# Kernel tuning notes

Hardware: AMD Instinct MI355X
Metric: run time of the kernel (lower is better)

Reference implementation:

```python
import jax, jax.numpy as jnp
import numpy as np

B, T = 256, 512
N_POS, N_ACT, H = 128, 64, 512
I = N_POS + N_ACT  # 192


def setup_inputs() -> dict:
    key = jax.random.key(0)
    ks = jax.random.split(key, 10)
    return {
        "observation": jax.random.normal(ks[0], (B, T, N_POS), jnp.float32),
        "action": jax.random.normal(ks[1], (B, T, N_ACT), jnp.float32),
        "h0": jax.random.normal(ks[2], (B, H), jnp.float32),
        "c0": jax.random.normal(ks[3], (B, H), jnp.float32),
        "W_ih": jax.random.normal(ks[4], (4 * H, I), jnp.float32) * 0.05,
        "W_hh": jax.random.normal(ks[5], (4 * H, H), jnp.float32) * 0.05,
        "b_ih": jax.random.normal(ks[6], (4 * H,), jnp.float32) * 0.05,
        "b_hh": jax.random.normal(ks[7], (4 * H,), jnp.float32) * 0.05,
        "W_out": jax.random.normal(ks[8], (1, H), jnp.float32) * 0.05,
        "b_out": jax.random.normal(ks[9], (1,), jnp.float32) * 0.05,
    }


def reference(observation, action, h0, c0, W_ih, W_hh, b_ih, b_hh, W_out, b_out):
    # x_t = cat([obs, act], -1): [B, T, I]
    x = jnp.concatenate([observation, action], axis=-1)
    # Precompute input-to-gate projection for all timesteps: [T, B, 4H]
    xg = jnp.swapaxes(jnp.einsum("bti,gi->btg", x, W_ih) + b_ih + b_hh, 0, 1)

    def step(carry, xg_t):
        h, c = carry
        gates = xg_t + h @ W_hh.T  # [B, 4H]
        i, f, g, o = jnp.split(gates, 4, axis=-1)  # PyTorch LSTMCell gate order
        i = jax.nn.sigmoid(i)
        f = jax.nn.sigmoid(f)
        g = jnp.tanh(g)
        o = jax.nn.sigmoid(o)
        c_new = f * c + i * g
        h_new = o * jnp.tanh(c_new)
        return (h_new, c_new), h_new

    (_, _), hs = jax.lax.scan(step, (h0, c0), xg)  # hs: [T, B, H]
    out = jnp.einsum("tbh,oh->tbo", hs, W_out) + b_out  # [T, B, 1]
    return jnp.swapaxes(out, 0, 1)  # [B, T, 1]
```

## Files before the change

### kernel.cpp

```cpp
#include <hip/hip_runtime.h>
#include <hip/hip_bf16.h>
#include <stdint.h>

#define BDIM 512

constexpr int Bb   = 256;
constexpr int Tt   = 512;
constexpr int Hh   = 512;
constexpr int NPOS = 128, NACT = 64, INPD = 192;
constexpr int NGRP = 8;
constexpr int BBr  = 32;
constexpr int NBLK = 32;
constexpr int HHd  = 16;
constexpr int KITH = Hh / 32;
constexpr int KITX = INPD / 32;
constexpr int HPAD = Hh + 8;
constexpr int XPAD = INPD + 8;
constexpr int GPAD = 68;

typedef __attribute__((ext_vector_type(8))) short short8;
typedef __attribute__((ext_vector_type(4))) float f32x4;
typedef __attribute__((ext_vector_type(4))) unsigned int u32x4;

__device__ __forceinline__ float bf2f(unsigned short u) {
  union { unsigned int i; float f; } v; v.i = ((unsigned int)u) << 16; return v.f;
}
__device__ __forceinline__ unsigned short f2bf(float f) {
  __hip_bfloat16 h = __float2bfloat16(f);
  return *reinterpret_cast<unsigned short*>(&h);
}
__device__ __forceinline__ float sigm(float x) { return 1.0f / (1.0f + __expf(-x)); }
__device__ __forceinline__ float tanh_fast(float x) {
  return 1.0f - 2.0f / (1.0f + __expf(2.0f * x));
}

__device__ __forceinline__ void store_wt16(void* p, u32x4 v) {
  asm volatile("global_store_dwordx4 %0, %1, off sc0 sc1" :: "v"(p), "v"(v) : "memory");
}
__device__ __forceinline__ u32x4 load_wt16(const void* p) {
  u32x4 r;
  asm volatile("global_load_dwordx4 %0, %1, off sc0 sc1" : "=v"(r) : "v"(p) : "memory");
  return r;
}
__device__ __forceinline__ void store_wt2(void* p, unsigned short v) {
  unsigned int w = v;
  asm volatile("global_store_short %0, %1, off sc0 sc1" :: "v"(p), "v"(w) : "memory");
}
__device__ __forceinline__ void store_wt4(void* p, unsigned int v) {
  asm volatile("global_store_dword %0, %1, off sc0 sc1" :: "v"(p), "v"(v) : "memory");
}
__device__ __forceinline__ unsigned int load_wt4(const void* p) {
  unsigned int r;
  asm volatile("global_load_dword %0, %1, off sc0 sc1" : "=v"(r) : "v"(p) : "memory");
  return r;
}
__device__ __forceinline__ void waitvm0() {
  asm volatile("s_waitcnt vmcnt(0)" ::: "memory");
}

__global__ void __launch_bounds__(BDIM, 2)
lstm_kernel(const float* __restrict__ obs, const float* __restrict__ actn,
            const float* __restrict__ h0, const float* __restrict__ c0,
            const float* __restrict__ W_ih, const float* __restrict__ W_hh,
            const float* __restrict__ b_ih, const float* __restrict__ b_hh,
            const float* __restrict__ W_out, const float* __restrict__ b_out,
            float* __restrict__ out, unsigned short* __restrict__ hbuf,
            unsigned int* __restrict__ flags)
{
  __shared__ __align__(16) unsigned short h_s[BBr * HPAD];
  __shared__ __align__(16) unsigned short x_s[BBr * XPAD];
  __shared__ float gates_s[BBr * GPAD];
  __shared__ float c_s[BBr * HHd];
  __shared__ float wout_s[Hh];
  __shared__ float bias_s[64];

  const int tid  = threadIdx.x;
  const int g    = blockIdx.x & 7;
  const int jb   = blockIdx.x >> 3;
  const int wv   = tid >> 6, lane = tid & 63;
  const int wm   = wv >> 2;
  const int wn   = wv & 3;
  const int cl   = lane & 15, qd = lane >> 4;

  unsigned short* hb0 = hbuf;
  unsigned short* hb1 = hbuf + (size_t)Bb * Hh;
  const size_t slotbase = (size_t)(g * NBLK + jb) * (BBr * HHd);
  const size_t grpbase  = (size_t)g * NBLK * (BBr * HHd);
  unsigned int* myflag = flags + (size_t)(g * NBLK + jb) * 32;
  const unsigned int* pollflag = flags + (size_t)(g * NBLK + (lane & 31)) * 32;

  short8 wfrag[KITH + KITX];
  {
    const int R = wn * Hh + jb * HHd + cl;
    const float* whh = W_hh + (size_t)R * Hh;
    const float* wih = W_ih + (size_t)R * INPD;
    #pragma unroll
    for (int kk = 0; kk < KITH + KITX; ++kk) {
      const int k0 = kk * 32 + qd * 8;
      short8 s;
      #pragma unroll
      for (int e = 0; e < 8; ++e) {
        const int k = k0 + e;
        const float f = (k < Hh) ? whh[k] : wih[k - Hh];
        s[e] = (short)f2bf(f);
      }
      wfrag[kk] = s;
    }
  }

  if (tid < 64) {
    const int R = (tid >> 4) * Hh + jb * HHd + (tid & 15);
    bias_s[tid] = b_ih[R] + b_hh[R];
  }
  for (int i = tid; i < Hh; i += BDIM) wout_s[i] = W_out[i];
  {
    const int m = tid >> 4, r = tid & 15;
    const size_t gi = (size_t)(g * BBr + m) * Hh + jb * HHd + r;
    c_s[tid] = c0[gi];
    store_wt2(hb0 + slotbase + tid, f2bf(h0[gi]));
  }
  const float bout = b_out[0];

  auto stage_x = [&](int t) {
    #pragma unroll
    for (int it = 0; it < 2; ++it) {
      const int i = tid + BDIM * it;
      const int m = i >> 5, c4 = i & 31;
      const float4 v = *(const float4*)(obs + ((size_t)(g * BBr + m) * Tt + t) * NPOS + c4 * 4);
      uint2 p;
      p.x = (unsigned)f2bf(v.x) | ((unsigned)f2bf(v.y) << 16);
      p.y = (unsigned)f2bf(v.z) | ((unsigned)f2bf(v.w) << 16);
      *(uint2*)(&x_s[m * XPAD + c4 * 4]) = p;
    }
    {
      const int m = tid >> 4, c4 = tid & 15;
      const float4 v = *(const float4*)(actn + ((size_t)(g * BBr + m) * Tt + t) * NACT + c4 * 4);
      uint2 p;
      p.x = (unsigned)f2bf(v.x) | ((unsigned)f2bf(v.y) << 16);
      p.y = (unsigned)f2bf(v.z) | ((unsigned)f2bf(v.w) << 16);
      *(uint2*)(&x_s[m * XPAD + NPOS + c4 * 4]) = p;
    }
  };
  auto xacc_compute = [&]() -> f32x4 {
    f32x4 a;
    { const float bv = bias_s[wn * 16 + cl]; a = (f32x4){bv, bv, bv, bv}; }
    const unsigned short* xrow = &x_s[(wm * 16 + cl) * XPAD + qd * 8];
    #pragma unroll
    for (int j = 0; j < KITX; ++j)
      a = __builtin_amdgcn_mfma_f32_16x16x32_bf16(*(const short8*)(xrow + j * 32),
                                                  wfrag[KITH + j], a, 0, 0, 0);
    return a;
  };
  auto poll = [&](unsigned int tgt) {
    if (tid < 64) {
      int spins = 0;
      for (;;) {
        const unsigned int v = load_wt4(pollflag);
        waitvm0();
        if (__all((int)(v >= tgt))) break;
        if (++spins > 3000000) break;
      }
    }
    __syncthreads();
  };

  waitvm0();
  __syncthreads();
  if (tid == 0) store_wt4(myflag, 1u);
  stage_x(0);
  __syncthreads();
  f32x4 xacc = xacc_compute();
  poll(1u);

  for (int t = 0; t < Tt; ++t) {
    const unsigned short* hsrc = (t & 1) ? hb1 : hb0;
    unsigned short* hdst       = (t & 1) ? hb0 : hb1;

    u32x4 hv[4];
    #pragma unroll
    for (int it = 0; it < 4; ++it) {
      const int i = tid + BDIM * it;
      hv[it] = load_wt16(hsrc + grpbase + (size_t)i * 8);
    }
    waitvm0();
    #pragma unroll
    for (int it = 0; it < 4; ++it) {
      const int i = tid + BDIM * it;
      *(u32x4*)(&h_s[((i >> 1) & 31) * HPAD + (i >> 6) * 16 + (i & 1) * 8]) = hv[it];
    }
    __syncthreads();

    f32x4 acc = xacc;
    const unsigned short* arow = &h_s[(wm * 16 + cl) * HPAD + qd * 8];
    #pragma unroll
    for (int kk = 0; kk < KITH; ++kk)
      acc = __builtin_amdgcn_mfma_f32_16x16x32_bf16(*(const short8*)(arow + kk * 32),
                                                    wfrag[kk], acc, 0, 0, 0);
    #pragma unroll
    for (int rg = 0; rg < 4; ++rg)
      gates_s[(wm * 16 + qd * 4 + rg) * GPAD + wn * 16 + cl] = acc[rg];
    __syncthreads();

    {
      const int m = tid >> 4, r = tid & 15;
      const float gi = gates_s[m * GPAD + r];
      const float gf = gates_s[m * GPAD + 16 + r];
      const float gg = gates_s[m * GPAD + 32 + r];
      const float go = gates_s[m * GPAD + 48 + r];
      const float cp = c_s[tid];
      const float iv = sigm(gi), fv = sigm(gf);
      const float gv = tanh_fast(gg), ov = sigm(go);
      const float cn = fv * cp + iv * gv;
      const float hn = ov * tanh_fast(cn);
      c_s[tid] = cn;
      store_wt2(hdst + slotbase + tid, f2bf(hn));
    }
    waitvm0();
    __syncthreads();
    if (tid == 0) store_wt4(myflag, (unsigned int)(t + 2));

    if (jb == 0 && t > 0 && tid < 256) {
      const int m = tid >> 3, l8 = tid & 7;
      const unsigned short* hr = &h_s[m * HPAD + l8 * 64];
      const float* wr = &wout_s[l8 * 64];
      float sum = 0.f;
      #pragma unroll 8
      for (int e = 0; e < 64; ++e) sum += bf2f(hr[e]) * wr[e];
      sum += __shfl_down(sum, 4, 64);
      sum += __shfl_down(sum, 2, 64);
      sum += __shfl_down(sum, 1, 64);
      if (l8 == 0) out[(size_t)(g * BBr + m) * Tt + (t - 1)] = sum + bout;
    }
    if (t + 1 < Tt) {
      stage_x(t + 1);
      __syncthreads();
      xacc = xacc_compute();
    } else {
      __syncthreads();
    }

    poll((unsigned int)(t + 2));
  }

  if (jb == 0 && tid < 256) {
    const int m = tid >> 3, l8 = tid & 7;
    u32x4 hvv[8];
    #pragma unroll
    for (int it = 0; it < 8; ++it) {
      const size_t a = grpbase + (size_t)((l8 * 4 + (it >> 1)) * BBr + m) * HHd + (it & 1) * 8;
      hvv[it] = load_wt16(hb0 + a);
    }
    waitvm0();
    float sum = 0.f;
    #pragma unroll
    for (int it = 0; it < 8; ++it) {
      const int d0 = l8 * 64 + (it >> 1) * 16 + (it & 1) * 8;
      #pragma unroll
      for (int j = 0; j < 4; ++j) {
        const unsigned u = hvv[it][j];
        sum += bf2f((unsigned short)(u & 0xffffu)) * wout_s[d0 + j * 2];
        sum += bf2f((unsigned short)(u >> 16))     * wout_s[d0 + j * 2 + 1];
      }
    }
    sum += __shfl_down(sum, 4, 64);
    sum += __shfl_down(sum, 2, 64);
    sum += __shfl_down(sum, 1, 64);
    if (l8 == 0) out[(size_t)(g * BBr + m) * Tt + (Tt - 1)] = sum + bout;
  }
}

extern "C" void kernel_launch(void* const* d_in, const int* in_sizes, int n_in,
                              void* d_out, int out_size, void* d_ws, size_t ws_size,
                              hipStream_t stream) {
  const float* obs   = (const float*)d_in[0];
  const float* actn  = (const float*)d_in[1];
  const float* h0    = (const float*)d_in[2];
  const float* c0    = (const float*)d_in[3];
  const float* W_ih  = (const float*)d_in[4];
  const float* W_hh  = (const float*)d_in[5];
  const float* b_ih  = (const float*)d_in[6];
  const float* b_hh  = (const float*)d_in[7];
  const float* W_out = (const float*)d_in[8];
  const float* b_out = (const float*)d_in[9];
  float* out = (float*)d_out;

  unsigned short* hbuf = (unsigned short*)d_ws;
  const size_t hbytes = (size_t)2 * Bb * Hh * sizeof(unsigned short);
  unsigned int* flags = (unsigned int*)((char*)d_ws + hbytes);

  hipMemsetAsync(flags, 0, 256 * 32 * sizeof(unsigned int), stream);

  hipFuncSetAttribute((const void*)lstm_kernel,
                      hipFuncAttributeMaxDynamicSharedMemorySize, 28672);
  hipLaunchKernelGGL(lstm_kernel, dim3(256), dim3(BDIM), 28672, stream,
                     obs, actn, h0, c0, W_ih, W_hh, b_ih, b_hh, W_out, b_out,
                     out, hbuf, flags);
}
```

Measured before the change: 1.944 ms.

## Regroup LSTM blocks per XCD and exchange hidden state through L2

Each block reads its XCC id and takes a rank from an atomic counter, so every batch group of 16 rows is spread over the 16 blocks on the same XCD. That allows hidden-state exchange and flag polling to use L2-coherent (sc0) accesses in place of device-scope ones. A token handshake at startup checks that the group really shares an L2 and falls back to device-scope accesses if not. Blocks now cover 16 batch rows by 32 hidden units, load x straight from global memory into MFMA fragments, and pack h stores into dwords. The cost is extra startup synchronisation and a reliance on how blocks are placed across XCDs.

New measurement: 2.587 ms. 33.1% more time.

```diff
diff --git a/kernel.cpp b/kernel.cpp
--- a/kernel.cpp
+++ b/kernel.cpp
@@ -8,15 +8,14 @@
 constexpr int Tt   = 512;
 constexpr int Hh   = 512;
 constexpr int NPOS = 128, NACT = 64, INPD = 192;
-constexpr int NGRP = 8;
-constexpr int BBr  = 32;
-constexpr int NBLK = 32;
-constexpr int HHd  = 16;
+constexpr int GBLK = 16;
+constexpr int RR   = 16;
+constexpr int HHd  = 32;
 constexpr int KITH = Hh / 32;
 constexpr int KITX = INPD / 32;
+constexpr int KIT  = KITH + KITX;
 constexpr int HPAD = Hh + 8;
-constexpr int XPAD = INPD + 8;
-constexpr int GPAD = 68;
+constexpr int GPAD = 132;
 
 typedef __attribute__((ext_vector_type(8))) short short8;
 typedef __attribute__((ext_vector_type(4))) float f32x4;
@@ -34,25 +33,35 @@
   return 1.0f - 2.0f / (1.0f + __expf(2.0f * x));
 }
 
-__device__ __forceinline__ void store_wt16(void* p, u32x4 v) {
-  asm volatile("global_store_dwordx4 %0, %1, off sc0 sc1" :: "v"(p), "v"(v) : "memory");
-}
-__device__ __forceinline__ u32x4 load_wt16(const void* p) {
+__device__ __forceinline__ u32x4 load_l2_16(const void* p) {
+  u32x4 r;
+  asm volatile("global_load_dwordx4 %0, %1, off sc0" : "=v"(r) : "v"(p) : "memory");
+  return r;
+}
+__device__ __forceinline__ unsigned int load_l2_4(const void* p) {
+  unsigned int r;
+  asm volatile("global_load_dword %0, %1, off sc0" : "=v"(r) : "v"(p) : "memory");
+  return r;
+}
+__device__ __forceinline__ void store_l2_4(void* p, unsigned int v) {
+  asm volatile("global_store_dword %0, %1, off sc0" :: "v"(p), "v"(v) : "memory");
+}
+__device__ __forceinline__ u32x4 load_dev16(const void* p) {
   u32x4 r;
   asm volatile("global_load_dwordx4 %0, %1, off sc0 sc1" : "=v"(r) : "v"(p) : "memory");
   return r;
 }
-__device__ __forceinline__ void store_wt2(void* p, unsigned short v) {
-  unsigned int w = v;
-  asm volatile("global_store_short %0, %1, off sc0 sc1" :: "v"(p), "v"(w) : "memory");
-}
-__device__ __forceinline__ void store_wt4(void* p, unsigned int v) {
-  asm volatile("global_store_dword %0, %1, off sc0 sc1" :: "v"(p), "v"(v) : "memory");
-}
-__device__ __forceinline__ unsigned int load_wt4(const void* p) {
+__device__ __forceinline__ unsigned int load_dev4(const void* p) {
   unsigned int r;
   asm volatile("global_load_dword %0, %1, off sc0 sc1" : "=v"(r) : "v"(p) : "memory");
   return r;
+}
+__device__ __forceinline__ void store_dev4(void* p, unsigned int v) {
+  asm volatile("global_store_dword %0, %1, off sc0 sc1" :: "v"(p), "v"(v) : "memory");
+}
+__device__ __forceinline__ void store_dev2(void* p, unsigned short v) {
+  unsigned int w = v;
+  asm volatile("global_store_short %0, %1, off sc0 sc1" :: "v"(p), "v"(w) : "memory");
 }
 __device__ __forceinline__ void waitvm0() {
   asm volatile("s_waitcnt vmcnt(0)" ::: "memory");
@@ -65,37 +74,112 @@
             const float* __restrict__ b_ih, const float* __restrict__ b_hh,
             const float* __restrict__ W_out, const float* __restrict__ b_out,
             float* __restrict__ out, unsigned short* __restrict__ hbuf,
-            unsigned int* __restrict__ flags)
+            unsigned int* __restrict__ flags, unsigned int* __restrict__ rankcnt,
+            unsigned int* __restrict__ grpbad, unsigned int* __restrict__ tok)
 {
-  __shared__ __align__(16) unsigned short h_s[BBr * HPAD];
-  __shared__ __align__(16) unsigned short x_s[BBr * XPAD];
-  __shared__ float gates_s[BBr * GPAD];
-  __shared__ float c_s[BBr * HHd];
+  __shared__ __align__(16) unsigned short h_s[RR * HPAD];
+  __shared__ float gates_s[RR * GPAD];
+  __shared__ float c_s[RR * HHd];
   __shared__ float wout_s[Hh];
-  __shared__ float bias_s[64];
+  __shared__ float bias_s[4 * HHd];
+  __shared__ int rank_sh;
+  __shared__ int okA_sh, okB_sh, dev_sh;
 
   const int tid  = threadIdx.x;
-  const int g    = blockIdx.x & 7;
-  const int jb   = blockIdx.x >> 3;
   const int wv   = tid >> 6, lane = tid & 63;
-  const int wm   = wv >> 2;
-  const int wn   = wv & 3;
   const int cl   = lane & 15, qd = lane >> 4;
+
+  unsigned int xcc;
+  asm volatile("s_getreg_b32 %0, hwreg(HW_REG_XCC_ID)" : "=s"(xcc));
+  xcc &= 7u;
+  if (tid == 0)
+    rank_sh = (int)__hip_atomic_fetch_add(rankcnt + (size_t)xcc * 32, 1u,
+                                          __ATOMIC_RELAXED, __HIP_MEMORY_SCOPE_AGENT);
+  __syncthreads();
+  const int rank = rank_sh;
+  const int g    = ((int)xcc * 2 + (rank >> 4)) & 15;
+  const int jb   = rank & 15;
 
   unsigned short* hb0 = hbuf;
   unsigned short* hb1 = hbuf + (size_t)Bb * Hh;
-  const size_t slotbase = (size_t)(g * NBLK + jb) * (BBr * HHd);
-  const size_t grpbase  = (size_t)g * NBLK * (BBr * HHd);
-  unsigned int* myflag = flags + (size_t)(g * NBLK + jb) * 32;
-  const unsigned int* pollflag = flags + (size_t)(g * NBLK + (lane & 31)) * 32;
-
-  short8 wfrag[KITH + KITX];
+  const size_t slotbase = (size_t)(g * GBLK + jb) * (RR * HHd);
+  const size_t grpbase  = (size_t)g * GBLK * (RR * HHd);
+  unsigned int* myflag = flags + (size_t)(g * GBLK + jb) * 32;
+  const unsigned int* pollflag = flags + (size_t)(g * GBLK + (lane & 15)) * 32;
+  unsigned int* mytok = tok + (size_t)(g * GBLK + jb) * 32;
+  const unsigned int TOKA = 0xA5000000u | (unsigned)(g << 8) | (unsigned)jb;
+  const unsigned int TOKB = 0x5A000000u | (unsigned)(g << 8) | (unsigned)jb;
+
+  auto pollv = [&](unsigned int tgt, bool dv, int valve) {
+    if (tid < 64) {
+      int spins = 0;
+      for (;;) {
+        const unsigned int v = dv ? load_dev4(pollflag) : load_l2_4(pollflag);
+        waitvm0();
+        if (__all((int)(v >= tgt))) break;
+        if (++spins > valve) break;
+      }
+    }
+    __syncthreads();
+  };
+  auto verify_read = [&](unsigned int expbase) -> void {
+    if (tid < 64) {
+      int good = 1;
+      if (lane < 16) {
+        const unsigned int v = load_l2_4(tok + (size_t)(g * GBLK + lane) * 32);
+        waitvm0();
+        good = (v == (expbase | (unsigned)(g << 8) | (unsigned)lane)) ? 1 : 0;
+      }
+      const int allg = __all(good);
+      if (lane == 0) { if (expbase == 0xA5000000u) okA_sh = allg; else okB_sh = allg; }
+    }
+  };
+
+  if (tid == 0) store_l2_4(mytok, TOKA);
   {
-    const int R = wn * Hh + jb * HHd + cl;
+    const int m = tid >> 5, r = tid & 31;
+    const size_t gi = (size_t)(g * RR + m) * Hh + jb * HHd + r;
+    c_s[tid] = c0[gi];
+    store_dev2(hb0 + slotbase + tid, f2bf(h0[gi]));
+  }
+  waitvm0();
+  __syncthreads();
+  if (tid == 0) store_dev4(myflag, 1u);
+  pollv(1u, true, 2000000);
+  verify_read(0xA5000000u);
+  __syncthreads();
+  if (tid == 0) store_dev4(myflag, 2u);
+  pollv(2u, true, 2000000);
+  if (tid == 0) {
+    store_l2_4(mytok, TOKB);
+    waitvm0();
+    store_dev4(myflag, 3u);
+  }
+  pollv(3u, true, 2000000);
+  verify_read(0x5A000000u);
+  __syncthreads();
+  if (tid == 0) {
+    if (!(okA_sh && okB_sh)) atomicOr(grpbad + (size_t)g * 32, 1u);
+    waitvm0();
+    store_dev4(myflag, 4u);
+  }
+  pollv(4u, true, 2000000);
+  if (tid == 0) {
+    const unsigned int gb = load_dev4(grpbad + (size_t)g * 32);
+    waitvm0();
+    dev_sh = (gb != 0);
+  }
+  __syncthreads();
+  const bool dev = (dev_sh != 0);
+
+  short8 wfrag[KIT];
+  {
+    const int L = wv * 16 + cl, q = L >> 5, r = L & 31;
+    const int R = q * Hh + jb * HHd + r;
     const float* whh = W_hh + (size_t)R * Hh;
     const float* wih = W_ih + (size_t)R * INPD;
     #pragma unroll
-    for (int kk = 0; kk < KITH + KITX; ++kk) {
+    for (int kk = 0; kk < KIT; ++kk) {
       const int k0 = kk * 32 + qd * 8;
       short8 s;
       #pragma unroll
@@ -107,119 +191,95 @@
       wfrag[kk] = s;
     }
   }
-
-  if (tid < 64) {
-    const int R = (tid >> 4) * Hh + jb * HHd + (tid & 15);
-    bias_s[tid] = b_ih[R] + b_hh[R];
-  }
-  for (int i = tid; i < Hh; i += BDIM) wout_s[i] = W_out[i];
-  {
-    const int m = tid >> 4, r = tid & 15;
-    const size_t gi = (size_t)(g * BBr + m) * Hh + jb * HHd + r;
-    c_s[tid] = c0[gi];
-    store_wt2(hb0 + slotbase + tid, f2bf(h0[gi]));
-  }
+  if (tid < 128) {
+    const int q = tid >> 5, r = tid & 31;
+    bias_s[tid] = b_ih[q * Hh + jb * HHd + r] + b_hh[q * Hh + jb * HHd + r];
+  }
+  wout_s[tid] = W_out[tid];
   const float bout = b_out[0];
 
-  auto stage_x = [&](int t) {
-    #pragma unroll
-    for (int it = 0; it < 2; ++it) {
-      const int i = tid + BDIM * it;
-      const int m = i >> 5, c4 = i & 31;
-      const float4 v = *(const float4*)(obs + ((size_t)(g * BBr + m) * Tt + t) * NPOS + c4 * 4);
-      uint2 p;
-      p.x = (unsigned)f2bf(v.x) | ((unsigned)f2bf(v.y) << 16);
-      p.y = (unsigned)f2bf(v.z) | ((unsigned)f2bf(v.w) << 16);
-      *(uint2*)(&x_s[m * XPAD + c4 * 4]) = p;
-    }
-    {
-      const int m = tid >> 4, c4 = tid & 15;
-      const float4 v = *(const float4*)(actn + ((size_t)(g * BBr + m) * Tt + t) * NACT + c4 * 4);
-      uint2 p;
-      p.x = (unsigned)f2bf(v.x) | ((unsigned)f2bf(v.y) << 16);
-      p.y = (unsigned)f2bf(v.z) | ((unsigned)f2bf(v.w) << 16);
-      *(uint2*)(&x_s[m * XPAD + NPOS + c4 * 4]) = p;
-    }
-  };
-  auto xacc_compute = [&]() -> f32x4 {
+  auto xacc_compute = [&](int t) -> f32x4 {
     f32x4 a;
-    { const float bv = bias_s[wn * 16 + cl]; a = (f32x4){bv, bv, bv, bv}; }
-    const unsigned short* xrow = &x_s[(wm * 16 + cl) * XPAD + qd * 8];
-    #pragma unroll
-    for (int j = 0; j < KITX; ++j)
-      a = __builtin_amdgcn_mfma_f32_16x16x32_bf16(*(const short8*)(xrow + j * 32),
-                                                  wfrag[KITH + j], a, 0, 0, 0);
+    { const float bv = bias_s[wv * 16 + cl]; a = (f32x4){bv, bv, bv, bv}; }
+    const int b = g * RR + cl;
+    const float* orow = obs  + ((size_t)b * Tt + t) * NPOS;
+    const float* arow = actn + ((size_t)b * Tt + t) * NACT;
+    #pragma unroll
+    for (int j = 0; j < KITX; ++j) {
+      const int k0 = j * 32 + qd * 8;
+      const float* src = (k0 < NPOS) ? (orow + k0) : (arow + (k0 - NPOS));
+      const float4 v0 = *(const float4*)src;
+      const float4 v1 = *(const float4*)(src + 4);
+      short8 s;
+      s[0] = (short)f2bf(v0.x); s[1] = (short)f2bf(v0.y);
+      s[2] = (short)f2bf(v0.z); s[3] = (short)f2bf(v0.w);
+      s[4] = (short)f2bf(v1.x); s[5] = (short)f2bf(v1.y);
+      s[6] = (short)f2bf(v1.z); s[7] = (short)f2bf(v1.w);
+      a = __builtin_amdgcn_mfma_f32_16x16x32_bf16(s, wfrag[KITH + j], a, 0, 0, 0);
+    }
     return a;
   };
-  auto poll = [&](unsigned int tgt) {
-    if (tid < 64) {
-      int spins = 0;
-      for (;;) {
-        const unsigned int v = load_wt4(pollflag);
-        waitvm0();
-        if (__all((int)(v >= tgt))) break;
-        if (++spins > 3000000) break;
-      }
-    }
-    __syncthreads();
-  };
-
-  waitvm0();
-  __syncthreads();
-  if (tid == 0) store_wt4(myflag, 1u);
-  stage_x(0);
-  __syncthreads();
-  f32x4 xacc = xacc_compute();
-  poll(1u);
+
+  f32x4 xacc = xacc_compute(0);
 
   for (int t = 0; t < Tt; ++t) {
     const unsigned short* hsrc = (t & 1) ? hb1 : hb0;
     unsigned short* hdst       = (t & 1) ? hb0 : hb1;
 
-    u32x4 hv[4];
-    #pragma unroll
-    for (int it = 0; it < 4; ++it) {
-      const int i = tid + BDIM * it;
-      hv[it] = load_wt16(hsrc + grpbase + (size_t)i * 8);
-    }
-    waitvm0();
-    #pragma unroll
-    for (int it = 0; it < 4; ++it) {
-      const int i = tid + BDIM * it;
-      *(u32x4*)(&h_s[((i >> 1) & 31) * HPAD + (i >> 6) * 16 + (i & 1) * 8]) = hv[it];
+    u32x4 hv0, hv1;
+    if (dev) {
+      hv0 = load_dev16(hsrc + grpbase + (size_t)tid * 8);
+      hv1 = load_dev16(hsrc + grpbase + (size_t)(tid + 512) * 8);
+    } else {
+      hv0 = load_l2_16(hsrc + grpbase + (size_t)tid * 8);
+      hv1 = load_l2_16(hsrc + grpbase + (size_t)(tid + 512) * 8);
+    }
+    waitvm0();
+    {
+      const int i0 = tid, i1 = tid + 512;
+      *(u32x4*)&h_s[((i0 & 63) >> 2) * HPAD + ((i0 >> 6) << 5) + ((i0 & 3) << 3)] = hv0;
+      *(u32x4*)&h_s[((i1 & 63) >> 2) * HPAD + ((i1 >> 6) << 5) + ((i1 & 3) << 3)] = hv1;
     }
     __syncthreads();
 
     f32x4 acc = xacc;
-    const unsigned short* arow = &h_s[(wm * 16 + cl) * HPAD + qd * 8];
+    const unsigned short* ar = &h_s[cl * HPAD + qd * 8];
     #pragma unroll
     for (int kk = 0; kk < KITH; ++kk)
-      acc = __builtin_amdgcn_mfma_f32_16x16x32_bf16(*(const short8*)(arow + kk * 32),
+      acc = __builtin_amdgcn_mfma_f32_16x16x32_bf16(*(const short8*)(ar + kk * 32),
                                                     wfrag[kk], acc, 0, 0, 0);
     #pragma unroll
     for (int rg = 0; rg < 4; ++rg)
-      gates_s[(wm * 16 + qd * 4 + rg) * GPAD + wn * 16 + cl] = acc[rg];
+      gates_s[(qd * 4 + rg) * GPAD + wv * 16 + cl] = acc[rg];
     __syncthreads();
 
     {
-      const int m = tid >> 4, r = tid & 15;
+      const int m = tid >> 5, r = tid & 31;
       const float gi = gates_s[m * GPAD + r];
-      const float gf = gates_s[m * GPAD + 16 + r];
-      const float gg = gates_s[m * GPAD + 32 + r];
-      const float go = gates_s[m * GPAD + 48 + r];
+      const float gf = gates_s[m * GPAD + HHd + r];
+      const float gg = gates_s[m * GPAD + 2 * HHd + r];
+      const float go = gates_s[m * GPAD + 3 * HHd + r];
       const float cp = c_s[tid];
       const float iv = sigm(gi), fv = sigm(gf);
       const float gv = tanh_fast(gg), ov = sigm(go);
       const float cn = fv * cp + iv * gv;
       const float hn = ov * tanh_fast(cn);
       c_s[tid] = cn;
-      store_wt2(hdst + slotbase + tid, f2bf(hn));
+      const unsigned int hb = (unsigned int)f2bf(hn);
+      const unsigned int hb2 = (unsigned int)__shfl_down((int)hb, 1, 64);
+      if ((tid & 1) == 0) {
+        if (dev) store_dev4(hdst + slotbase + tid, hb | (hb2 << 16));
+        else     store_l2_4(hdst + slotbase + tid, hb | (hb2 << 16));
+      }
     }
     waitvm0();
     __syncthreads();
-    if (tid == 0) store_wt4(myflag, (unsigned int)(t + 2));
-
-    if (jb == 0 && t > 0 && tid < 256) {
+    if (tid == 0) {
+      if (dev) store_dev4(myflag, (unsigned int)(t + 5));
+      else     store_l2_4(myflag, (unsigned int)(t + 5));
+    }
+
+    if (jb == 0 && t > 0 && tid < 128) {
       const int m = tid >> 3, l8 = tid & 7;
       const unsigned short* hr = &h_s[m * HPAD + l8 * 64];
       const float* wr = &wout_s[l8 * 64];
@@ -229,43 +289,32 @@
       sum += __shfl_down(sum, 4, 64);
       sum += __shfl_down(sum, 2, 64);
       sum += __shfl_down(sum, 1, 64);
-      if (l8 == 0) out[(size_t)(g * BBr + m) * Tt + (t - 1)] = sum + bout;
-    }
-    if (t + 1 < Tt) {
-      stage_x(t + 1);
-      __syncthreads();
-      xacc = xacc_compute();
-    } else {
-      __syncthreads();
-    }
-
-    poll((unsigned int)(t + 2));
-  }
-
-  if (jb == 0 && tid < 256) {
+      if (l8 == 0) out[(size_t)(g * RR + m) * Tt + (t - 1)] = sum + bout;
+    }
+    if (t + 1 < Tt) xacc = xacc_compute(t + 1);
+
+    pollv((unsigned int)(t + 5), dev, 200000);
+  }
+
+  if (jb == 0 && tid < 128) {
     const int m = tid >> 3, l8 = tid & 7;
-    u32x4 hvv[8];
+    float sum = 0.f;
     #pragma unroll
     for (int it = 0; it < 8; ++it) {
-      const size_t a = grpbase + (size_t)((l8 * 4 + (it >> 1)) * BBr + m) * HHd + (it & 1) * 8;
-      hvv[it] = load_wt16(hb0 + a);
-    }
-    waitvm0();
-    float sum = 0.f;
-    #pragma unroll
-    for (int it = 0; it < 8; ++it) {
-      const int d0 = l8 * 64 + (it >> 1) * 16 + (it & 1) * 8;
+      const int d = l8 * 64 + it * 8;
+      const void* p = hb0 + grpbase + (size_t)(d >> 5) * (RR * HHd) + m * HHd + (d & 31);
+      const u32x4 v = dev ? load_dev16(p) : load_l2_16(p);
+      waitvm0();
       #pragma unroll
-      for (int j = 0; j < 4; ++j) {
-        const unsigned u = hvv[it][j];
-        sum += bf2f((unsigned short)(u & 0xffffu)) * wout_s[d0 + j * 2];
-        sum += bf2f((unsigned short)(u >> 16))     * wout_s[d0 + j * 2 + 1];
+      for (int j2 = 0; j2 < 4; ++j2) {
+        sum += bf2f((unsigned short)(v[j2] & 0xffffu)) * wout_s[d + j2 * 2];
+        sum += bf2f((unsigned short)(v[j2] >> 16))     * wout_s[d + j2 * 2 + 1];
       }
     }
     sum += __shfl_down(sum, 4, 64);
     sum += __shfl_down(sum, 2, 64);
     sum += __shfl_down(sum, 1, 64);
-    if (l8 == 0) out[(size_t)(g * BBr + m) * Tt + (Tt - 1)] = sum + bout;
+    if (l8 == 0) out[(size_t)(g * RR + m) * Tt + (Tt - 1)] = sum + bout;
   }
 }
 
@@ -285,14 +334,17 @@
   float* out = (float*)d_out;
 
   unsigned short* hbuf = (unsigned short*)d_ws;
-  const size_t hbytes = (size_t)2 * Bb * Hh * sizeof(unsigned short);
-  unsigned int* flags = (unsigned int*)((char*)d_ws + hbytes);
-
-  hipMemsetAsync(flags, 0, 256 * 32 * sizeof(unsigned int), stream);
+  char* p = (char*)d_ws + (size_t)2 * Bb * Hh * sizeof(unsigned short);
+  unsigned int* flags   = (unsigned int*)p;
+  unsigned int* rankcnt = (unsigned int*)(p + 32768);
+  unsigned int* grpbad  = (unsigned int*)(p + 32768 + 1024);
+  unsigned int* tokp    = (unsigned int*)(p + 32768 + 1024 + 2048);
+
+  hipMemsetAsync(p, 0, 32768 + 1024 + 2048 + 32768, stream);
 
   hipFuncSetAttribute((const void*)lstm_kernel,
-                      hipFuncAttributeMaxDynamicSharedMemorySize, 28672);
-  hipLaunchKernelGGL(lstm_kernel, dim3(256), dim3(BDIM), 28672, stream,
+                      hipFuncAttributeMaxDynamicSharedMemorySize, 53248);
+  hipLaunchKernelGGL(lstm_kernel, dim3(256), dim3(BDIM), 53248, stream,
                      obs, actn, h0, c0, W_ih, W_hh, b_ih, b_hh, W_out, b_out,
-                     out, hbuf, flags);
-}
+                     out, hbuf, flags, rankcnt, grpbad, tokp);
+}
```
